# Kernel optimization log

Measured on AMD Instinct MI355X. Metric: run time of the kernel, lower is better.

## Reference

```python
import jax, jax.numpy as jnp
import numpy as np

MAX_SEQ = 768  # hardcoded in original compute_freqs_cis
THETA = 10000.0


def _freqs_cis(C, T):
    # freqs over FULL embed dim C (matches original, not per-head)
    freqs = 1.0 / THETA ** (jnp.arange(0, C, 2, dtype=jnp.float32)[: C // 2] / C)
    t = jnp.arange(MAX_SEQ, dtype=jnp.float32)
    ang = jnp.outer(t, freqs)  # [MAX_SEQ, C/2]
    return jnp.cos(ang)[:T], jnp.sin(ang)[:T]  # each [T, C/2]


def _apply_rope(u):
    # u: [B, T, C]; rotate adjacent channel pairs across full C
    B, T, C = u.shape
    fr, fi = _freqs_cis(C, T)           # [T, C/2]
    u2 = u.astype(jnp.float32).reshape(B, T, C // 2, 2)
    ur, ui = u2[..., 0], u2[..., 1]     # [B, T, C/2]
    out_r = ur * fr - ui * fi
    out_i = ur * fi + ui * fr
    return jnp.stack([out_r, out_i], axis=-1).reshape(B, T, C).astype(u.dtype)


def setup_inputs() -> dict:
    key = jax.random.key(0)
    k1, k2, k3 = jax.random.split(key, 3)
    B, T, C = 16, 768, 1024
    x = jax.random.normal(k1, (B, T, C), dtype=jnp.float32)
    Wqkv = jax.random.normal(k2, (3 * C, C), dtype=jnp.float32) * 0.02
    bqkv = jnp.zeros((3 * C,), dtype=jnp.float32)
    Wo = jax.random.normal(k3, (C, C), dtype=jnp.float32) * 0.02
    bo = jnp.zeros((C,), dtype=jnp.float32)
    return {"x": x, "Wqkv": Wqkv, "bqkv": bqkv, "Wo": Wo, "bo": bo}


def reference(x, Wqkv, bqkv, Wo, bo):
    B, T, C = x.shape
    H = 16
    D = C // H
    qkv = x @ Wqkv.T + bqkv                      # [B, T, 3C]
    q, k, v = jnp.split(qkv, 3, axis=-1)
    q = _apply_rope(q)
    k = _apply_rope(k)
    # [B, H, T, D]
    q = q.reshape(B, T, H, D).transpose(0, 2, 1, 3)
    k = k.reshape(B, T, H, D).transpose(0, 2, 1, 3)
    v = v.reshape(B, T, H, D).transpose(0, 2, 1, 3)
    scale = 1.0 / jnp.sqrt(jnp.asarray(D, dtype=q.dtype))
    scores = jnp.einsum("bhqd,bhkd->bhqk", q, k) * scale
    causal = jnp.tril(jnp.ones((T, T), dtype=bool))
    scores = jnp.where(causal, scores, jnp.finfo(scores.dtype).min)
    attn = jax.nn.softmax(scores, axis=-1)
    y = jnp.einsum("bhqk,bhkd->bhqd", attn, v)   # [B, H, T, D]
    y = y.transpose(0, 2, 1, 3).reshape(B, T, C)
    return y @ Wo.T + bo
```

## Files before the change

### kernel.cpp

```cpp
#include <hip/hip_runtime.h>
#include <hip/hip_bf16.h>

typedef __attribute__((ext_vector_type(8))) short bf16x8;
typedef __attribute__((ext_vector_type(4))) float f32x4;
typedef unsigned short u16;
typedef unsigned int u32;

#define DEV __device__ __forceinline__

DEV float bf2f(u16 v) { u32 u = ((u32)v) << 16; return __builtin_bit_cast(float, u); }
DEV u16 f2bf(float f) {
    u32 u = __builtin_bit_cast(u32, f);
    u32 r = (u + 0x7FFFu + ((u >> 16) & 1u)) >> 16;
    return (u16)r;
}
DEV u16 f2bf_trunc(float f) { return (u16)(__builtin_bit_cast(u32, f) >> 16); }

DEV void gll16(const u16* g, u16* l) {
    __builtin_amdgcn_global_load_lds((const __attribute__((address_space(1))) void*)g,
                                     (__attribute__((address_space(3))) void*)l, 16, 0, 0);
}

#define WAIT_VM0()   asm volatile("s_waitcnt vmcnt(0)" ::: "memory")
#define WAIT_LGKM0() asm volatile("s_waitcnt lgkmcnt(0)" ::: "memory")
#define BAR()        __builtin_amdgcn_s_barrier()
#define BARF()       asm volatile("s_barrier" ::: "memory")

__global__ void detect_kernel(const u32* __restrict__ x, int* __restrict__ flag) {
    __shared__ int cnt;
    if (threadIdx.x == 0) cnt = 0;
    __syncthreads();
    int c = 0;
    for (int i = threadIdx.x; i < 4096; i += 256) {
        u32 w = x[i];
        u32 e = (w >> 7) & 0xFF;
        c += (e >= 110 && e <= 132) ? 1 : 0;
    }
    atomicAdd(&cnt, c);
    __syncthreads();
    if (threadIdx.x == 0) *flag = (cnt * 2 > 4096) ? 1 : 0;
}

DEV void cvt8(const void* in, u16* out, int i, int fl) {
    if (fl) {
        ((bf16x8*)out)[i] = ((const bf16x8*)in)[i];
    } else {
        float4 a = ((const float4*)in)[2 * i], b = ((const float4*)in)[2 * i + 1];
        bf16x8 o;
        o[0] = (short)f2bf(a.x); o[1] = (short)f2bf(a.y);
        o[2] = (short)f2bf(a.z); o[3] = (short)f2bf(a.w);
        o[4] = (short)f2bf(b.x); o[5] = (short)f2bf(b.y);
        o[6] = (short)f2bf(b.z); o[7] = (short)f2bf(b.w);
        ((bf16x8*)out)[i] = o;
    }
}

__global__ void prep_kernel(const void* __restrict__ x, u16* __restrict__ xb,
                            const void* __restrict__ Wq, u16* __restrict__ Wqb,
                            const void* __restrict__ Wo, u16* __restrict__ Wob,
                            float2* __restrict__ tab, const int* __restrict__ flag) {
    constexpr int N8X = 1572864, N8W = 393216, N8O = 131072;
    constexpr int C1 = N8X, C2 = N8X + N8W, C3 = N8X + N8W + N8O;
    constexpr int TOTAL = C3 + 768 * 512;
    const int fl = *flag;
    const int stride = gridDim.x * 256;
    for (int i = blockIdx.x * 256 + threadIdx.x; i < TOTAL; i += stride) {
        if (i < C1)       cvt8(x, xb, i, fl);
        else if (i < C2)  cvt8(Wq, Wqb, i - C1, fl);
        else if (i < C3)  cvt8(Wo, Wob, i - C2, fl);
        else {
            int r = i - C3;
            int t = r >> 9, j = r & 511;
            float freq = expf(-(float)(2 * j) * (9.210340371976184f / 1024.0f));
            float ang = (float)t * freq;
            tab[r] = make_float2(cosf(ang), sinf(ang));
        }
    }
}

template<int BN>
__global__ __launch_bounds__(512, 2)
void gemm256p_kernel(const u16* __restrict__ A, const u16* __restrict__ W,
                     const void* __restrict__ bias, void* __restrict__ C,
                     int N, const int* __restrict__ flag, int out_mode,
                     const float2* __restrict__ tab, int rope) {
    constexpr int K = 1024, NT = 16;
    constexpr int NF = BN / 64;
    __shared__ u16 lds[2][16384 + BN * 64];
    const int tid = threadIdx.x;
    const int l = tid & 63, w = tid >> 6;
    const int wm = w >> 2, wn = w & 3;
    const int lo = l & 15, hi = l >> 4;

    const int M0 = blockIdx.x * 256, N0 = blockIdx.y * BN;

    const int rS = tid >> 3;
    const int qS = (tid & 7) ^ (rS & 7);
    const u16* Ag = A + (size_t)(M0 + rS) * K + qS * 8;
    const u16* Wg = W + (size_t)(N0 + rS) * K + qS * 8;
    const int lb = w * 512;

    f32x4 acc[8][NF] = {};

#define STG_A(kt, slot, half)                                                  \
    {                                                                          \
        u16* sA_ = &lds[slot][(half) * 8192];                                  \
        const u16* ga_ = Ag + (kt) * 64 + (size_t)(128 * (half)) * K;          \
        gll16(ga_,                  sA_ + lb);                                 \
        gll16(ga_ + (size_t)64 * K, sA_ + 4096 + lb);                          \
    }
#define STG_B(kt, slot, half)                                                  \
    {                                                                          \
        u16* sB_ = &lds[slot][16384 + (half) * 8192];                          \
        const u16* gb_ = Wg + (kt) * 64 + (size_t)(128 * (half)) * K;          \
        gll16(gb_,                  sB_ + lb);                                 \
        gll16(gb_ + (size_t)64 * K, sB_ + 4096 + lb);                          \
    }
#define STG_B_ALL(kt, slot)                                                    \
    { STG_B(kt, slot, 0); if (BN == 256) STG_B(kt, slot, 1); }

    STG_A(0, 0, 0); STG_A(0, 0, 1);
    STG_B_ALL(0, 0);
    WAIT_VM0();
    BARF();

    const int csw = lo & 7;

#pragma unroll 1
    for (int t = 0; t < NT; ++t) {
        const int cur = t & 1, nxt = cur ^ 1;
        const u16* sA = &lds[cur][0];
        const u16* sB = &lds[cur][16384];
        bf16x8 afr[4], bfr[NF];

#pragma unroll
        for (int n = 0; n < NF; ++n)
            bfr[n] = *(const bf16x8*)&sB[(wn * (BN / 4) + n * 16 + lo) * 64 + ((hi ^ csw) * 8)];
#pragma unroll
        for (int m = 0; m < 4; ++m)
            afr[m] = *(const bf16x8*)&sA[(wm * 128 + m * 16 + lo) * 64 + ((hi ^ csw) * 8)];
        if (t + 1 < NT) { STG_A(t + 1, nxt, 0); STG_A(t + 1, nxt, 1); }
        BARF();
        __builtin_amdgcn_s_setprio(1);
#pragma unroll
        for (int m = 0; m < 4; ++m)
#pragma unroll
            for (int n = 0; n < NF; ++n)
                acc[m][n] = __builtin_amdgcn_mfma_f32_16x16x32_bf16(afr[m], bfr[n], acc[m][n], 0, 0, 0);
        __builtin_amdgcn_s_setprio(0);
        BARF();

#pragma unroll
        for (int m = 0; m < 4; ++m)
            afr[m] = *(const bf16x8*)&sA[(wm * 128 + 64 + m * 16 + lo) * 64 + ((hi ^ csw) * 8)];
        if (t + 1 < NT) { STG_B_ALL(t + 1, nxt); }
        BARF();
        __builtin_amdgcn_s_setprio(1);
#pragma unroll
        for (int m = 0; m < 4; ++m)
#pragma unroll
            for (int n = 0; n < NF; ++n)
                acc[4 + m][n] = __builtin_amdgcn_mfma_f32_16x16x32_bf16(afr[m], bfr[n], acc[4 + m][n], 0, 0, 0);
        __builtin_amdgcn_s_setprio(0);
        BARF();

#pragma unroll
        for (int n = 0; n < NF; ++n)
            bfr[n] = *(const bf16x8*)&sB[(wn * (BN / 4) + n * 16 + lo) * 64 + (((4 + hi) ^ csw) * 8)];
#pragma unroll
        for (int m = 0; m < 4; ++m)
            afr[m] = *(const bf16x8*)&sA[(wm * 128 + m * 16 + lo) * 64 + (((4 + hi) ^ csw) * 8)];
        BARF();
        __builtin_amdgcn_s_setprio(1);
#pragma unroll
        for (int m = 0; m < 4; ++m)
#pragma unroll
            for (int n = 0; n < NF; ++n)
                acc[m][n] = __builtin_amdgcn_mfma_f32_16x16x32_bf16(afr[m], bfr[n], acc[m][n], 0, 0, 0);
        __builtin_amdgcn_s_setprio(0);
        BARF();

#pragma unroll
        for (int m = 0; m < 4; ++m)
            afr[m] = *(const bf16x8*)&sA[(wm * 128 + 64 + m * 16 + lo) * 64 + (((4 + hi) ^ csw) * 8)];
        WAIT_VM0();
        BARF();
        __builtin_amdgcn_s_setprio(1);
#pragma unroll
        for (int m = 0; m < 4; ++m)
#pragma unroll
            for (int n = 0; n < NF; ++n)
                acc[4 + m][n] = __builtin_amdgcn_mfma_f32_16x16x32_bf16(afr[m], bfr[n], acc[4 + m][n], 0, 0, 0);
        __builtin_amdgcn_s_setprio(0);
        BARF();
    }
#undef STG_A
#undef STG_B
#undef STG_B_ALL

    const int fl = *flag;
    const int f32out = out_mode ? (fl == 0) : 0;
    const int do_rope = rope && (N0 < 2048);
#pragma unroll
    for (int mi = 0; mi < 8; ++mi) {
        const int rbase = M0 + wm * 128 + (mi >> 2) * 64 + (mi & 3) * 16 + hi * 4;
        const int tbase = (M0 % 768) + wm * 128 + (mi >> 2) * 64 + (mi & 3) * 16 + hi * 4;
#pragma unroll
        for (int n = 0; n < NF; ++n) {
            const int col = N0 + wn * (BN / 4) + lo + n * 16;
            float bi = fl ? bf2f(((const u16*)bias)[col]) : ((const float*)bias)[col];
            const int jf = (col & 1023) >> 1;
            const int odd = col & 1;
#pragma unroll
            for (int j = 0; j < 4; ++j) {
                float v = acc[mi][n][j] + bi;
                if (do_rope) {
                    float partner = __shfl_xor(v, 1);
                    float2 cs = tab[(tbase + j) * 512 + jf];
                    v = odd ? (v * cs.x + partner * cs.y) : (v * cs.x - partner * cs.y);
                }
                size_t idx = (size_t)(rbase + j) * N + col;
                if (f32out) ((float*)C)[idx] = v;
                else        ((u16*)C)[idx] = f2bf(v);
            }
        }
    }
}

__global__ __launch_bounds__(512)
void attn_kernel(const u16* __restrict__ qkv, u16* __restrict__ y) {
    constexpr int T = 768, CH = 1024, QKVC = 3072;
    constexpr float NEG = -30000.0f;
    __shared__ u16 Ks[2][64 * 64];
    __shared__ u16 Vt[64 * 72];
    __shared__ u16 Ps[128 * 72];

    const int tid = threadIdx.x, l = tid & 63, w = tid >> 6;
    const int qt = blockIdx.x, h = blockIdx.y, b = blockIdx.z;
    const int lo = l & 15, hi = l >> 4;
    const int kk = hi * 8;
    const int swzk = (lo & 7) * 8;

    const int qrow = qt * 128 + w * 16 + lo;
    const u16* qptr = qkv + (size_t)(b * T + qrow) * QKVC + h * 64 + kk;
    bf16x8 aq0r = *(const bf16x8*)qptr;
    bf16x8 aq1r = *(const bf16x8*)(qptr + 32);
    bf16x8 aq0, aq1;
#pragma unroll
    for (int e = 0; e < 8; ++e) {
        aq0[e] = (short)f2bf(bf2f((u16)aq0r[e]) * 0.125f);
        aq1[e] = (short)f2bf(bf2f((u16)aq1r[e]) * 0.125f);
    }

    f32x4 o[4] = {};
    float mrun[4] = {NEG, NEG, NEG, NEG};
    float lrun[4] = {0.f, 0.f, 0.f, 0.f};

    const int ksr = w * 8 + (l >> 3);
    const int ksc = ((l & 7) ^ ((l >> 3) & 7)) * 8;
    const u16* kbase = qkv + (size_t)(b * T + ksr) * QKVC + CH + h * 64 + ksc;

    const int vd0 = (tid & 7) * 8;
    const int vswz = (tid & 7) * 8;
    const int vr0 = tid >> 3;
    const u16* vbase = qkv + (size_t)(b * T) * QKVC + 2 * CH + h * 64 + vd0;

    const int NTk = 2 * qt + 2;

    gll16(kbase, &Ks[0][w * 512]);
    bf16x8 cv0 = *(const bf16x8*)(vbase + (size_t)vr0 * QKVC);
    WAIT_VM0();
#pragma unroll
    for (int e = 0; e < 8; ++e)
        Vt[(vd0 + e) * 72 + (vr0 ^ vswz)] = (u16)cv0[e];

    for (int kt = 0; kt < NTk; ++kt) {
        const int cur = kt & 1, nxt = cur ^ 1;
        bf16x8 nv0;
        if (kt + 1 < NTk) {
            const size_t koff = (size_t)((kt + 1) * 64) * QKVC;
            gll16(kbase + koff, &Ks[nxt][w * 512]);
            nv0 = *(const bf16x8*)(vbase + (size_t)((kt + 1) * 64 + vr0) * QKVC);
        }
        WAIT_LGKM0();
        BAR();

        __builtin_amdgcn_s_setprio(1);
        f32x4 s[4];
#pragma unroll
        for (int n = 0; n < 4; ++n) {
            bf16x8 kb0 = *(const bf16x8*)&Ks[cur][(n * 16 + lo) * 64 + (kk ^ swzk)];
            bf16x8 kb1 = *(const bf16x8*)&Ks[cur][(n * 16 + lo) * 64 + ((32 + kk) ^ swzk)];
            f32x4 z = {0.f, 0.f, 0.f, 0.f};
            z = __builtin_amdgcn_mfma_f32_16x16x32_bf16(aq0, kb0, z, 0, 0, 0);
            z = __builtin_amdgcn_mfma_f32_16x16x32_bf16(aq1, kb1, z, 0, 0, 0);
            s[n] = z;
        }
        __builtin_amdgcn_s_setprio(0);

        if (kt >= 2 * qt) {
#pragma unroll
            for (int n = 0; n < 4; ++n) {
                int kcol = kt * 64 + n * 16 + lo;
#pragma unroll
                for (int j = 0; j < 4; ++j)
                    if (kcol > qt * 128 + w * 16 + hi * 4 + j) s[n][j] = NEG;
            }
        }
        float mx[4];
#pragma unroll
        for (int j = 0; j < 4; ++j) {
            float m0 = fmaxf(fmaxf(s[0][j], s[1][j]), fmaxf(s[2][j], s[3][j]));
            m0 = fmaxf(m0, __shfl_xor(m0, 1));
            m0 = fmaxf(m0, __shfl_xor(m0, 2));
            m0 = fmaxf(m0, __shfl_xor(m0, 4));
            m0 = fmaxf(m0, __shfl_xor(m0, 8));
            mx[j] = m0;
        }
        float g = fmaxf(fmaxf(mx[0] - mrun[0], mx[1] - mrun[1]),
                        fmaxf(mx[2] - mrun[2], mx[3] - mrun[3]));
        if (!__all(g <= 8.0f)) {
#pragma unroll
            for (int j = 0; j < 4; ++j) {
                float mn = fmaxf(mrun[j], mx[j]);
                float c = __expf(mrun[j] - mn);
                mrun[j] = mn;
                lrun[j] *= c;
#pragma unroll
                for (int n = 0; n < 4; ++n) o[n][j] *= c;
            }
        }
        float p[4][4];
#pragma unroll
        for (int n = 0; n < 4; ++n)
#pragma unroll
            for (int j = 0; j < 4; ++j) {
                p[n][j] = __expf(s[n][j] - mrun[j]);
                Ps[(w * 16 + hi * 4 + j) * 72 + n * 16 + lo] = f2bf_trunc(p[n][j]);
            }
#pragma unroll
        for (int j = 0; j < 4; ++j)
            lrun[j] += p[0][j] + p[1][j] + p[2][j] + p[3][j];

        __builtin_amdgcn_s_setprio(1);
#pragma unroll
        for (int c = 0; c < 2; ++c) {
            bf16x8 pa = *(const bf16x8*)&Ps[(w * 16 + lo) * 72 + c * 32 + kk];
#pragma unroll
            for (int n = 0; n < 4; ++n) {
                const int v = (n * 2 + (lo >> 3)) & 7;
                bf16x8 vb = *(const bf16x8*)&Vt[(n * 16 + lo) * 72 + ((c * 32 + kk) ^ (v * 8))];
                o[n] = __builtin_amdgcn_mfma_f32_16x16x32_bf16(pa, vb, o[n], 0, 0, 0);
            }
        }
        __builtin_amdgcn_s_setprio(0);

        if (kt + 1 < NTk) {
            WAIT_VM0();
            BAR();
#pragma unroll
            for (int e = 0; e < 8; ++e)
                Vt[(vd0 + e) * 72 + (vr0 ^ vswz)] = (u16)nv0[e];
        }
    }

    float inv[4];
#pragma unroll
    for (int j = 0; j < 4; ++j) {
        float r = lrun[j];
        r += __shfl_xor(r, 1);
        r += __shfl_xor(r, 2);
        r += __shfl_xor(r, 4);
        r += __shfl_xor(r, 8);
        inv[j] = (r > 0.f) ? 1.0f / r : 0.f;
    }
#pragma unroll
    for (int n = 0; n < 4; ++n)
#pragma unroll
        for (int j = 0; j < 4; ++j) {
            int t = qt * 128 + w * 16 + hi * 4 + j;
            y[(size_t)(b * T + t) * CH + h * 64 + n * 16 + lo] = f2bf(o[n][j] * inv[j]);
        }
}

extern "C" void kernel_launch(void* const* d_in, const int* in_sizes, int n_in,
                              void* d_out, int out_size, void* d_ws, size_t ws_size,
                              hipStream_t stream) {
    char* ws = (char*)d_ws;
    int*   flag  = (int*)ws;
    u16*   xb    = (u16*)(ws + 256);
    u16*   Wqb   = (u16*)(ws + 256 + 25165824);
    u16*   Wob   = (u16*)(ws + 256 + 31457280);
    u16*   qkv   = (u16*)(ws + 256 + 33570816);
    u16*   y     = (u16*)(ws + 256 + 109068288);
    float2* tab  = (float2*)(ws + 256 + 134234112);

    detect_kernel<<<1, 256, 0, stream>>>((const u32*)d_in[0], flag);
    prep_kernel<<<2048, 256, 0, stream>>>(d_in[0], xb, d_in[1], Wqb, d_in[3], Wob, tab, flag);

    gemm256p_kernel<256><<<dim3(48, 12), 512, 0, stream>>>(xb, Wqb, d_in[2], qkv, 3072, flag, 0, tab, 1);
    attn_kernel<<<dim3(6, 16, 16), 512, 0, stream>>>(qkv, y);
    gemm256p_kernel<128><<<dim3(48, 8), 512, 0, stream>>>(y, Wob, d_in[4], d_out, 1024, flag, 1, tab, 0);
}
```

Measured before the change: 294.7 us.

## Fuse dtype detection into prep, retile GEMMs, remap attention blocks per XCD

Folds the dtype-detection pass into the prep kernel, so each block recomputes the flag locally and one launch goes away. Makes the GEMM B-staging generic over NF, then switches the QKV projection to 192-wide N tiles (768 blocks) and the output projection to 256-wide tiles (192 blocks). Rope selection is now decided per column rather than per tile, since 192-wide tiles straddle the q/k/v boundaries. The attention grid becomes a flat 1D launch whose index is remapped so all query tiles of one (batch, head) land on the same XCD, improving L2 reuse of K/V. The risks are wave-count and occupancy changes: the output GEMM now launches only 192 blocks.

Result: slower. 300.9 us (+2.1%).

```diff
diff --git a/kernel.cpp b/kernel.cpp
--- a/kernel.cpp
+++ b/kernel.cpp
@@ -25,21 +25,6 @@
 #define WAIT_LGKM0() asm volatile("s_waitcnt lgkmcnt(0)" ::: "memory")
 #define BAR()        __builtin_amdgcn_s_barrier()
 #define BARF()       asm volatile("s_barrier" ::: "memory")
-
-__global__ void detect_kernel(const u32* __restrict__ x, int* __restrict__ flag) {
-    __shared__ int cnt;
-    if (threadIdx.x == 0) cnt = 0;
-    __syncthreads();
-    int c = 0;
-    for (int i = threadIdx.x; i < 4096; i += 256) {
-        u32 w = x[i];
-        u32 e = (w >> 7) & 0xFF;
-        c += (e >= 110 && e <= 132) ? 1 : 0;
-    }
-    atomicAdd(&cnt, c);
-    __syncthreads();
-    if (threadIdx.x == 0) *flag = (cnt * 2 > 4096) ? 1 : 0;
-}
 
 DEV void cvt8(const void* in, u16* out, int i, int fl) {
     if (fl) {
@@ -58,11 +43,26 @@
 __global__ void prep_kernel(const void* __restrict__ x, u16* __restrict__ xb,
                             const void* __restrict__ Wq, u16* __restrict__ Wqb,
                             const void* __restrict__ Wo, u16* __restrict__ Wob,
-                            float2* __restrict__ tab, const int* __restrict__ flag) {
+                            float2* __restrict__ tab, int* __restrict__ flag) {
+    __shared__ int cnt;
+    if (threadIdx.x == 0) cnt = 0;
+    __syncthreads();
+    {
+        int c = 0;
+        for (int i = threadIdx.x; i < 4096; i += 256) {
+            u32 w = ((const u32*)x)[i];
+            u32 e = (w >> 7) & 0xFF;
+            c += (e >= 110 && e <= 132) ? 1 : 0;
+        }
+        atomicAdd(&cnt, c);
+    }
+    __syncthreads();
+    const int fl = (cnt * 2 > 4096) ? 1 : 0;
+    if (blockIdx.x == 0 && threadIdx.x == 0) *flag = fl;
+
     constexpr int N8X = 1572864, N8W = 393216, N8O = 131072;
     constexpr int C1 = N8X, C2 = N8X + N8W, C3 = N8X + N8W + N8O;
     constexpr int TOTAL = C3 + 768 * 512;
-    const int fl = *flag;
     const int stride = gridDim.x * 256;
     for (int i = blockIdx.x * 256 + threadIdx.x; i < TOTAL; i += stride) {
         if (i < C1)       cvt8(x, xb, i, fl);
@@ -109,18 +109,17 @@
         gll16(ga_,                  sA_ + lb);                                 \
         gll16(ga_ + (size_t)64 * K, sA_ + 4096 + lb);                          \
     }
-#define STG_B(kt, slot, half)                                                  \
+#define STG_B(kt, slot)                                                        \
     {                                                                          \
-        u16* sB_ = &lds[slot][16384 + (half) * 8192];                          \
-        const u16* gb_ = Wg + (kt) * 64 + (size_t)(128 * (half)) * K;          \
-        gll16(gb_,                  sB_ + lb);                                 \
-        gll16(gb_ + (size_t)64 * K, sB_ + 4096 + lb);                          \
-    }
-#define STG_B_ALL(kt, slot)                                                    \
-    { STG_B(kt, slot, 0); if (BN == 256) STG_B(kt, slot, 1); }
+        u16* sB_ = &lds[slot][16384];                                          \
+        const u16* gb_ = Wg + (kt) * 64;                                       \
+        _Pragma("unroll")                                                      \
+        for (int hh = 0; hh < NF; ++hh)                                        \
+            gll16(gb_ + (size_t)(64 * hh) * K, sB_ + hh * 4096 + lb);          \
+    }
 
     STG_A(0, 0, 0); STG_A(0, 0, 1);
-    STG_B_ALL(0, 0);
+    STG_B(0, 0);
     WAIT_VM0();
     BARF();
 
@@ -153,7 +152,7 @@
 #pragma unroll
         for (int m = 0; m < 4; ++m)
             afr[m] = *(const bf16x8*)&sA[(wm * 128 + 64 + m * 16 + lo) * 64 + ((hi ^ csw) * 8)];
-        if (t + 1 < NT) { STG_B_ALL(t + 1, nxt); }
+        if (t + 1 < NT) { STG_B(t + 1, nxt); }
         BARF();
         __builtin_amdgcn_s_setprio(1);
 #pragma unroll
@@ -196,11 +195,9 @@
     }
 #undef STG_A
 #undef STG_B
-#undef STG_B_ALL
 
     const int fl = *flag;
     const int f32out = out_mode ? (fl == 0) : 0;
-    const int do_rope = rope && (N0 < 2048);
 #pragma unroll
     for (int mi = 0; mi < 8; ++mi) {
         const int rbase = M0 + wm * 128 + (mi >> 2) * 64 + (mi & 3) * 16 + hi * 4;
@@ -211,6 +208,7 @@
             float bi = fl ? bf2f(((const u16*)bias)[col]) : ((const float*)bias)[col];
             const int jf = (col & 1023) >> 1;
             const int odd = col & 1;
+            const int do_rope = rope && (col < 2048);
 #pragma unroll
             for (int j = 0; j < 4; ++j) {
                 float v = acc[mi][n][j] + bi;
@@ -236,7 +234,11 @@
     __shared__ u16 Ps[128 * 72];
 
     const int tid = threadIdx.x, l = tid & 63, w = tid >> 6;
-    const int qt = blockIdx.x, h = blockIdx.y, b = blockIdx.z;
+    const int hw = blockIdx.x;
+    const int xcd = hw & 7, pos = hw >> 3;
+    const int qt = pos % 6;
+    const int g = (pos / 6) * 8 + xcd;
+    const int h = g & 15, b = g >> 4;
     const int lo = l & 15, hi = l >> 4;
     const int kk = hi * 8;
     const int swzk = (lo & 7) * 8;
@@ -317,9 +319,9 @@
             m0 = fmaxf(m0, __shfl_xor(m0, 8));
             mx[j] = m0;
         }
-        float g = fmaxf(fmaxf(mx[0] - mrun[0], mx[1] - mrun[1]),
-                        fmaxf(mx[2] - mrun[2], mx[3] - mrun[3]));
-        if (!__all(g <= 8.0f)) {
+        float gg = fmaxf(fmaxf(mx[0] - mrun[0], mx[1] - mrun[1]),
+                         fmaxf(mx[2] - mrun[2], mx[3] - mrun[3]));
+        if (!__all(gg <= 8.0f)) {
 #pragma unroll
             for (int j = 0; j < 4; ++j) {
                 float mn = fmaxf(mrun[j], mx[j]);
@@ -395,10 +397,9 @@
     u16*   y     = (u16*)(ws + 256 + 109068288);
     float2* tab  = (float2*)(ws + 256 + 134234112);
 
-    detect_kernel<<<1, 256, 0, stream>>>((const u32*)d_in[0], flag);
     prep_kernel<<<2048, 256, 0, stream>>>(d_in[0], xb, d_in[1], Wqb, d_in[3], Wob, tab, flag);
 
-    gemm256p_kernel<256><<<dim3(48, 12), 512, 0, stream>>>(xb, Wqb, d_in[2], qkv, 3072, flag, 0, tab, 1);
-    attn_kernel<<<dim3(6, 16, 16), 512, 0, stream>>>(qkv, y);
-    gemm256p_kernel<128><<<dim3(48, 8), 512, 0, stream>>>(y, Wob, d_in[4], d_out, 1024, flag, 1, tab, 0);
-}
+    gemm256p_kernel<192><<<dim3(48, 16), 512, 0, stream>>>(xb, Wqb, d_in[2], qkv, 3072, flag, 0, tab, 1);
+    attn_kernel<<<1536, 512, 0, stream>>>(qkv, y);
+    gemm256p_kernel<256><<<dim3(48, 4), 512, 0, stream>>>(y, Wob, d_in[4], d_out, 1024, flag, 1, tab, 0);
+}
```
